# Performance work log

Hardware: AMD Instinct MI355X
Metric: run time of the kernel (lower is better)

The kernel has to match this reference:

```python
import jax, jax.numpy as jnp
import numpy as np

B, CIN, NH, W, L, K = 16, 64, 64, 32, 4, 5
EPS = 1e-5
FORGET_BIAS = 1.0


def conv(x, w, b=None):
    # x: [B,C,H,W], w: [O,I,k,k] -> SAME padding, stride 1 (NCHW)
    y = jax.lax.conv_general_dilated(x, w, (1, 1), 'SAME',
                                     dimension_numbers=('NCHW', 'OIHW', 'NCHW'))
    if b is not None:
        y = y + b[None, :, None, None]
    return y


def ln(x, g, b):
    # torch LayerNorm([C,W,W]): normalize each sample over (C,H,W)
    m = jnp.mean(x, axis=(1, 2, 3), keepdims=True)
    v = jnp.mean((x - m) ** 2, axis=(1, 2, 3), keepdims=True)
    return (x - m) * jax.lax.rsqrt(v + EPS) * g[None] + b[None]


def attn_channel(q, kv):
    # q: [B,C,W,H], kv: [B,L,C,W,H]
    b, c, w, h = q.shape
    qf = q.reshape(b, c, w * h)                 # [B,C,HW]
    kf = kv.reshape(b, -1, w * h)               # [B,L*C,HW]
    a = jax.nn.softmax(jnp.einsum('bcp,blp->bcl', qf, kf), axis=2)  # [B,C,L*C]
    out = jnp.einsum('bcl,blp->bcp', a, kf)     # [B,C,HW]
    return out.reshape(b, c, w, h)


def attn_spatial(q, kv):
    # q: [B,C,W,H], kv: [B,L,C,W,H]
    b, c, w, h = q.shape
    qf = q.reshape(b, c, w * h).transpose(0, 2, 1)          # [B,HW,C]
    kf = kv.transpose(0, 1, 3, 4, 2).reshape(b, -1, c)      # [B,L*HW,C]
    a = jax.nn.softmax(jnp.einsum('bpc,bqc->bpq', qf, kf), axis=2)  # [B,HW,L*HW]
    out = jnp.einsum('bpq,bqc->bpc', a, kf)                 # [B,HW,C]
    return out.reshape(b, w, h, c).transpose(0, 3, 1, 2)


def setup_inputs() -> dict:
    key = jax.random.key(0)
    ks = iter(jax.random.split(key, 64))
    rn = lambda shape, s=1.0: jax.random.normal(next(ks), shape, jnp.float32) * s
    ones = lambda shape: jnp.ones(shape, jnp.float32)
    zeros = lambda shape: jnp.zeros(shape, jnp.float32)
    s = 0.02
    d = {}
    d['x_t'] = rn((B, CIN, W, W))
    d['h_t'] = rn((B, NH, W, W))
    d['c_t'] = rn((B, NH, W, W))
    d['c_historys'] = rn((B, L, NH, W, W))
    d['m_t'] = rn((B, NH, W, W))
    d['w_x'] = rn((7 * NH, CIN, K, K), s); d['ln_x_g'] = ones((7 * NH, W, W)); d['ln_x_b'] = zeros((7 * NH, W, W))
    d['w_h'] = rn((4 * NH, NH, K, K), s);  d['ln_h_g'] = ones((4 * NH, W, W)); d['ln_h_b'] = zeros((4 * NH, W, W))
    d['w_m'] = rn((3 * NH, NH, K, K), s);  d['ln_m_g'] = ones((3 * NH, W, W)); d['ln_m_b'] = zeros((3 * NH, W, W))
    d['w_o'] = rn((NH, 2 * NH, K, K), s);  d['ln_o_g'] = ones((NH, W, W));     d['ln_o_b'] = zeros((NH, W, W))
    d['w_last'] = rn((NH, 2 * NH, 1, 1), s)
    d['s_norm_g'] = ones((NH, W, W)); d['s_norm_b'] = zeros((NH, W, W))
    d['c_norm_g'] = ones((NH, W, W)); d['c_norm_b'] = zeros((NH, W, W))
    d['ca_w1'] = rn((NH, NH, K, K), s); d['ca_b1'] = zeros((NH,))
    d['ca_ln_g'] = ones((NH, W, W));    d['ca_ln_b'] = zeros((NH, W, W))
    d['ca_w2'] = rn((NH, NH, 1, 1), s); d['ca_b2'] = zeros((NH,))
    d['sa_w1'] = rn((NH, NH, K, K), s)
    d['sa_ln_g'] = ones((NH, W, W));    d['sa_ln_b'] = zeros((NH, W, W))
    d['sa_w2'] = rn((NH, NH, 1, 1), s)
    d['attn_w'] = rn((NH, NH, 1, 1), s)
    return d


def reference(x_t, h_t, c_t, c_historys, m_t,
              w_x, ln_x_g, ln_x_b, w_h, ln_h_g, ln_h_b, w_m, ln_m_g, ln_m_b,
              w_o, ln_o_g, ln_o_b, w_last,
              s_norm_g, s_norm_b, c_norm_g, c_norm_b,
              ca_w1, ca_b1, ca_ln_g, ca_ln_b, ca_w2, ca_b2,
              sa_w1, sa_ln_g, sa_ln_b, sa_w2, attn_w):
    x_concat = ln(conv(x_t, w_x), ln_x_g, ln_x_b)
    h_concat = ln(conv(h_t, w_h), ln_h_g, ln_h_b)
    m_concat = ln(conv(m_t, w_m), ln_m_g, ln_m_b)
    (i_x, f_x, g_x, i_xp, f_xp, g_xp, o_x) = jnp.split(x_concat, 7, axis=1)
    (i_h, f_h, g_h, o_h) = jnp.split(h_concat, 4, axis=1)
    (i_m, f_m, g_m) = jnp.split(m_concat, 3, axis=1)

    i_t = jax.nn.sigmoid(i_x + i_h)
    f_t = jax.nn.sigmoid(f_x + f_h + FORGET_BIAS)
    g_t = jnp.tanh(g_x + g_h)

    # attn_sum_fussion(c_t, query=f_t, keys=c_historys, values=c_historys)
    sp = ln(c_t + attn_spatial(f_t, c_historys), s_norm_g, s_norm_b)
    ch = ln(c_t + attn_channel(f_t, c_historys), c_norm_g, c_norm_b)
    s_a = conv(jax.nn.relu(ln(conv(sp, sa_w1), sa_ln_g, sa_ln_b)), sa_w2)
    c_a = conv(jax.nn.relu(ln(conv(ch, ca_w1, ca_b1), ca_ln_g, ca_ln_b)), ca_w2, ca_b2)
    attn = conv(s_a + c_a, attn_w)
    c_new = attn + i_t * g_t

    i_tp = jax.nn.sigmoid(i_xp + i_m)
    f_tp = jax.nn.sigmoid(f_xp + f_m + FORGET_BIAS)
    g_tp = jnp.tanh(g_xp + g_m)
    m_new = f_tp * m_t + i_tp * g_tp

    mem = jnp.concatenate((c_new, m_new), axis=1)
    o_t = jax.nn.sigmoid(o_x + o_h + ln(conv(mem, w_o), ln_o_g, ln_o_b))
    h_new = o_t * jnp.tanh(conv(mem, w_last))
    return h_new, c_new, m_new
```

## Files before the change

kernel.cpp:

```cpp
#include <hip/hip_runtime.h>
#include <hip/hip_bf16.h>

#define N1 (1u << 20)

typedef __attribute__((ext_vector_type(8))) short s8v;
typedef __attribute__((ext_vector_type(4))) float f4v;

static __device__ __forceinline__ float sigm(float x){ return 1.f/(1.f + __expf(-x)); }
static __device__ __forceinline__ float tanh_(float x){ return 1.f - 2.f/(__expf(2.f*x) + 1.f); }

static __device__ __forceinline__ ushort f2b(float f){
  union { float f; uint u; } x; x.f = f;
  uint r = x.u + 0x7FFFu + ((x.u >> 16) & 1u);
  return (ushort)(r >> 16);
}

static __device__ __forceinline__ void red_atomic2(float s, float q, float* d, int b, int t){
  #pragma unroll
  for (int m = 32; m; m >>= 1){ s += __shfl_xor(s, m); q += __shfl_xor(q, m); }
  if ((t & 63) == 0){ atomicAdd(&d[b*2], s); atomicAdd(&d[b*2+1], q); }
}

__global__ void k_zero(float* __restrict__ p){ p[threadIdx.x] = 0.f; }

__global__ __launch_bounds__(256) void k_wprep3(
    const float* __restrict__ sA, ushort* __restrict__ dA, int CoA, int CiA, int nA,
    const float* __restrict__ sB, ushort* __restrict__ dB, int CoB, int CiB, int nB,
    const float* __restrict__ sC, ushort* __restrict__ dC, int CoC, int CiC, int nC)
{
  int idx = blockIdx.x*256 + threadIdx.x;
  const float* s; ushort* d; int Co, Ci;
  if (idx < nA){ s=sA; d=dA; Co=CoA; Ci=CiA; }
  else if ((idx -= nA) < nB){ s=sB; d=dB; Co=CoB; Ci=CiB; }
  else if ((idx -= nB) < nC){ s=sC; d=dC; Co=CoC; Ci=CiC; }
  else return;
  int ci = idx % Ci; int r = idx / Ci; int co = r % Co; int tap = r / Co;
  d[idx] = f2b(s[((size_t)(co*Ci + ci))*25 + tap]);
}

struct PT { const float* s; ushort* d; const float* st; const float* g; const float* bb; };

__global__ __launch_bounds__(256) void k_prepT3(PT ja, PT jb, PT jc, int n0, int n1, float invN)
{
  const int lp = blockIdx.y;
  PT j; int pl;
  if (lp < n0){ j = ja; pl = lp; }
  else if (lp < n0 + n1){ j = jb; pl = lp - n0; }
  else { j = jc; pl = lp - n0 - n1; }
  const float* sp = j.s + ((size_t)pl << 16);
  float mean = 0.f, rstd = 0.f;
  if (j.st){
    float s0 = j.st[pl*2], s1 = j.st[pl*2+1];
    mean = s0*invN; rstd = rsqrtf(s1*invN - mean*mean + 1e-5f);
  }
  const int p0 = blockIdx.x << 6;
  __shared__ __align__(16) float T[64][68];
  const int t = threadIdx.x, c = t >> 2, g4 = t & 3;
  #pragma unroll
  for (int i = 0; i < 4; ++i){
    const int px = (g4 << 4) + (i << 2);
    float4 f = *(const float4*)(sp + ((size_t)c << 10) + p0 + px);
    if (j.st){
      const size_t li = ((size_t)c << 10) + p0 + px;
      float4 gv = *(const float4*)(j.g + li);
      float4 bv = *(const float4*)(j.bb + li);
      f.x = (f.x - mean)*rstd*gv.x + bv.x;
      f.y = (f.y - mean)*rstd*gv.y + bv.y;
      f.z = (f.z - mean)*rstd*gv.z + bv.z;
      f.w = (f.w - mean)*rstd*gv.w + bv.w;
    }
    *(float4*)&T[c][px] = f;
  }
  __syncthreads();
  const int p = t >> 2, c0 = (t & 3) << 4;
  uint w4[8];
  #pragma unroll
  for (int k = 0; k < 8; ++k){
    ushort lo = f2b(T[c0 + 2*k][p]);
    ushort hi = f2b(T[c0 + 2*k + 1][p]);
    w4[k] = (uint)lo | ((uint)hi << 16);
  }
  ushort* dst = j.d + ((((size_t)pl << 10) + p0 + p) << 6) + c0;
  *(uint4*)(dst)     = *(uint4*)&w4[0];
  *(uint4*)(dst + 8) = *(uint4*)&w4[4];
}

__global__ __launch_bounds__(256) void k_prepTm(const float* __restrict__ src, ushort* __restrict__ dT)
{
  const int lp = blockIdx.y;
  const int p0 = blockIdx.x << 6;
  const float* sp = src + ((size_t)lp << 16);
  __shared__ __align__(16) float T[64][68];
  const int t = threadIdx.x, c = t >> 2, g4 = t & 3;
  #pragma unroll
  for (int i = 0; i < 4; ++i){
    const int px = (g4 << 4) + (i << 2);
    *(float4*)&T[c][px] = *(const float4*)(sp + ((size_t)c << 10) + p0 + px);
  }
  __syncthreads();
  const int p = t >> 2, c0 = (t & 3) << 4;
  uint w4[8];
  #pragma unroll
  for (int k = 0; k < 8; ++k)
    w4[k] = (uint)f2b(T[c0 + 2*k][p]) | ((uint)f2b(T[c0 + 2*k + 1][p]) << 16);
  ushort* dst = dT + ((((size_t)(lp >> 1) << 10) + p0 + p) << 7) + ((lp & 1) << 6) + c0;
  *(uint4*)(dst)     = *(uint4*)&w4[0];
  *(uint4*)(dst + 8) = *(uint4*)&w4[4];
}

struct Seg {
  const ushort* inT; const ushort* w; const float* bias;
  float* out; float* ostat;
  int Cin, Cout;
};
struct Segs3 { Seg s[3]; int b1, b2; };

template<int MT>
__global__ __launch_bounds__(256, MT==4 ? 2 : 3) void k_convX(Segs3 Sg)
{
  constexpr int CO   = MT*16;
  constexpr int NW   = 5*CO*4;
  constexpr int ITW  = (NW + 255) / 256;
  constexpr int DXSH = (MT == 4 ? 8 : 7);

  const int b = blockIdx.y;
  const int cog = blockIdx.x >> 2, pxblk = blockIdx.x & 3;
  const int si = (cog >= Sg.b1) + (cog >= Sg.b2);
  const Seg sg = Sg.s[si];
  const int base = si == 0 ? 0 : (si == 1 ? Sg.b1 : Sg.b2);
  const int co0 = (cog - base) * CO;
  const int r0 = pxblk << 3;
  const int t = threadIdx.x, w = t >> 6, l = t & 63;
  const int lane16 = l & 15, quad = l >> 4;

  __shared__ __align__(16) ushort S_[4][12][36][8];
  __shared__ __align__(16) ushort W_[2][5*CO*32];

  f4v acc[MT][4];
  #pragma unroll
  for (int mi = 0; mi < MT; ++mi)
    #pragma unroll
    for (int n = 0; n < 4; ++n) acc[mi][n] = (f4v){0.f,0.f,0.f,0.f};

  size_t woff0[ITW];
  #pragma unroll
  for (int it = 0; it < ITW; ++it){
    const int u = t + it*256;
    const int l16u = u & 15, qu = (u >> 4) & 3;
    const int miu = (u >> 6) & (MT - 1), dxu = u >> DXSH;
    woff0[it] = ((size_t)(dxu*sg.Cout + co0 + miu*16 + l16u))*sg.Cin + (qu << 3);
  }
  const size_t wdy = (size_t)5 * sg.Cout * sg.Cin;

  const int ncc = sg.Cin >> 5;
  for (int cc = 0; cc < ncc; ++cc){
    __syncthreads();
    for (int idx = t; idx < 432; idx += 256){
      const int row = idx / 36, col = idx - row*36;
      const int ir = r0 - 2 + row, ic = col - 2;
      uint4 pk[4] = {make_uint4(0,0,0,0),make_uint4(0,0,0,0),make_uint4(0,0,0,0),make_uint4(0,0,0,0)};
      if ((unsigned)ir < 32u && (unsigned)ic < 32u){
        const ushort* bp = sg.inT + ((size_t)((b << 10) + (ir << 5) + ic)) * sg.Cin + (cc << 5);
        #pragma unroll
        for (int q = 0; q < 4; ++q) pk[q] = *(const uint4*)(bp + (q << 3));
      }
      #pragma unroll
      for (int q = 0; q < 4; ++q) *(uint4*)&S_[q][row][col][0] = pk[q];
    }
    {
      uint4 wreg[ITW];
      #pragma unroll
      for (int it = 0; it < ITW; ++it)
        if (ITW*256 == NW || t + it*256 < NW)
          wreg[it] = *(const uint4*)(sg.w + woff0[it] + (cc << 5));
      #pragma unroll
      for (int it = 0; it < ITW; ++it)
        if (ITW*256 == NW || t + it*256 < NW)
          *(uint4*)&W_[0][(size_t)(t + it*256) * 8] = wreg[it];
    }
    __syncthreads();
    #pragma unroll
    for (int dy = 0; dy < 5; ++dy){
      uint4 nreg[ITW];
      if (dy < 4){
        #pragma unroll
        for (int it = 0; it < ITW; ++it)
          if (ITW*256 == NW || t + it*256 < NW)
            nreg[it] = *(const uint4*)(sg.w + woff0[it] + (size_t)(dy+1)*wdy + (cc << 5));
      }
      #pragma unroll
      for (int dx = 0; dx < 5; ++dx){
        s8v a[MT];
        #pragma unroll
        for (int mi = 0; mi < MT; ++mi){
          const int au = ((((dx*MT + mi) << 2) + quad) << 4) + lane16;
          a[mi] = *(const s8v*)&W_[dy & 1][au << 3];
        }
        #pragma unroll
        for (int n = 0; n < 4; ++n){
          const int srow = (w << 1) + (n >> 1) + dy;
          const int col = ((n & 1) << 4) + lane16 + dx;
          s8v bb = *(const s8v*)&S_[quad][srow][col][0];
          #pragma unroll
          for (int mi = 0; mi < MT; ++mi)
            acc[mi][n] = __builtin_amdgcn_mfma_f32_16x16x32_bf16(a[mi], bb, acc[mi][n], 0, 0, 0);
        }
      }
      if (dy < 4){
        #pragma unroll
        for (int it = 0; it < ITW; ++it)
          if (ITW*256 == NW || t + it*256 < NW)
            *(uint4*)&W_[(dy+1) & 1][(size_t)(t + it*256) * 8] = nreg[it];
      }
      __syncthreads();
    }
  }
  float lsum = 0.f, lsq = 0.f;
  #pragma unroll
  for (int mi = 0; mi < MT; ++mi){
    const int co = co0 + mi*16 + (quad << 2);
    #pragma unroll
    for (int n = 0; n < 4; ++n){
      const int row = r0 + (w << 1) + (n >> 1);
      const int col = ((n & 1) << 4) + lane16;
      #pragma unroll
      for (int i = 0; i < 4; ++i){
        float v = acc[mi][n][i] + (sg.bias ? sg.bias[co+i] : 0.f);
        sg.out[(((size_t)(b*sg.Cout + co + i)) << 10) + (row << 5) + col] = v;
        lsum += v; lsq += v*v;
      }
    }
  }
  if (sg.ostat) red_atomic2(lsum, lsq, sg.ostat, b, t);
}

__global__ __launch_bounds__(256) void k_prep(const float* __restrict__ src,
                                              ushort* __restrict__ outC,
                                              ushort* __restrict__ outT)
{
  const int plane = blockIdx.y;
  const int p0 = blockIdx.x << 6;
  const float* sp = src + ((size_t)plane << 16);
  __shared__ __align__(16) float T[64][68];
  const int t = threadIdx.x, c = t >> 2, g = t & 3;
  #pragma unroll
  for (int i = 0; i < 4; ++i){
    float4 f = *(const float4*)(sp + ((size_t)c << 10) + p0 + (g << 4) + (i << 2));
    *(float4*)&T[c][(g << 4) + (i << 2)] = f;
    if (outC){
      uint2 pk2;
      pk2.x = (uint)f2b(f.x) | ((uint)f2b(f.y) << 16);
      pk2.y = (uint)f2b(f.z) | ((uint)f2b(f.w) << 16);
      *(uint2*)(outC + ((((size_t)plane << 6) + c) << 10) + p0 + (g << 4) + (i << 2)) = pk2;
    }
  }
  __syncthreads();
  const int p = t >> 2, c0 = (t & 3) << 4;
  uint w4[8];
  #pragma unroll
  for (int k = 0; k < 8; ++k){
    ushort lo = f2b(T[c0 + 2*k][p]);
    ushort hi = f2b(T[c0 + 2*k + 1][p]);
    w4[k] = (uint)lo | ((uint)hi << 16);
  }
  ushort* dst = outT + ((((size_t)plane << 10) + p0 + p) << 6) + c0;
  *(uint4*)(dst)     = *(uint4*)&w4[0];
  *(uint4*)(dst + 8) = *(uint4*)&w4[4];
}

__global__ __launch_bounds__(256) void k_gates(
    const float* __restrict__ bufx, const float* __restrict__ bufh, const float* __restrict__ bufm,
    const float* __restrict__ lnxg, const float* __restrict__ lnxb,
    const float* __restrict__ lnhg, const float* __restrict__ lnhb,
    const float* __restrict__ lnmg, const float* __restrict__ lnmb,
    const float* __restrict__ m_t, const float* __restrict__ stats,
    float* __restrict__ ft, float* __restrict__ ig, float* __restrict__ osum,
    float* __restrict__ memo, float* __restrict__ out_m)
{
  const int idx = blockIdx.x*256 + threadIdx.x;
  const int b = idx >> 16, rem = idx & 65535;
  const int c = rem >> 10, p = rem & 1023;

  float mx = stats[b*2]      * (1.f/458752.f);
  float vx = stats[b*2+1]    * (1.f/458752.f) - mx*mx;  float rx = rsqrtf(vx + 1e-5f);
  float mh = stats[32+b*2]   * (1.f/262144.f);
  float vh = stats[32+b*2+1] * (1.f/262144.f) - mh*mh;  float rh = rsqrtf(vh + 1e-5f);
  float mm = stats[64+b*2]   * (1.f/196608.f);
  float vm = stats[64+b*2+1] * (1.f/196608.f) - mm*mm;  float rm = rsqrtf(vm + 1e-5f);

  auto LX = [&](int k){
    size_t ch = (size_t)k*64 + c; size_t gi = ((size_t)b*448 + ch)*1024 + p; size_t li = ch*1024 + p;
    return (bufx[gi] - mx)*rx*lnxg[li] + lnxb[li]; };
  auto LH = [&](int k){
    size_t ch = (size_t)k*64 + c; size_t gi = ((size_t)b*256 + ch)*1024 + p; size_t li = ch*1024 + p;
    return (bufh[gi] - mh)*rh*lnhg[li] + lnhb[li]; };
  auto LM = [&](int k){
    size_t ch = (size_t)k*64 + c; size_t gi = ((size_t)b*192 + ch)*1024 + p; size_t li = ch*1024 + p;
    return (bufm[gi] - mm)*rm*lnmg[li] + lnmb[li]; };

  float i_t = sigm(LX(0) + LH(0));
  float f_t = sigm(LX(1) + LH(1) + 1.f);
  float g_t = tanh_(LX(2) + LH(2));
  float i_p = sigm(LX(3) + LM(0));
  float f_p = sigm(LX(4) + LM(1) + 1.f);
  float g_p = tanh_(LX(5) + LM(2));
  float ox = LX(6), oh = LH(3);

  ft[idx]   = f_t;
  ig[idx]   = i_t * g_t;
  osum[idx] = ox + oh;
  float mn = f_p * m_t[idx] + i_p * g_p;
  out_m[idx] = mn;
  memo[((size_t)(b*128 + 64 + c) << 10) + p] = mn;
}

__global__ __launch_bounds__(256) void k_spat_mfma(
    const ushort* __restrict__ qT, const ushort* __restrict__ kvC, const ushort* __restrict__ kvT,
    const float* __restrict__ c_t, float* __restrict__ sp_raw, float* __restrict__ stats)
{
  const int p0 = blockIdx.x << 6, b = blockIdx.y;
  const int t = threadIdx.x, w = t >> 6, l = t & 63;
  const int lane16 = l & 15, quad = l >> 4;
  __shared__ __align__(16) ushort Kt[64][72];
  __shared__ __align__(16) ushort Kc[64][72];
  __shared__ __align__(16) ushort Eb[64][72];
  __shared__ __align__(16) float  XO[64][65];

  s8v qa0, qa1;
  {
    const ushort* qr = qT + ((((size_t)b << 10) + p0 + (w << 4) + lane16) << 6) + (quad << 3);
    qa0 = *(const s8v*)(qr);
    qa1 = *(const s8v*)(qr + 32);
  }
  f4v o0 = {0.f,0.f,0.f,0.f}, o1 = o0, o2 = o0, o3 = o0, dacc = o0;
  const short oneb = (short)0x3F80;
  const s8v ones = { oneb, oneb, oneb, oneb, oneb, oneb, oneb, oneb };

  const int r = t >> 2, g4 = (t & 3) << 4;
  for (int chunk = 0; chunk < 64; ++chunk){
    const int lidx = chunk >> 4, pk = (chunk & 15) << 6;
    __syncthreads();
    {
      const ushort* sc = kvC + ((((size_t)(b*4 + lidx) << 6) + r) << 10) + pk + g4;
      *(uint4*)&Kc[r][g4]     = *(const uint4*)(sc);
      *(uint4*)&Kc[r][g4 + 8] = *(const uint4*)(sc + 8);
      const ushort* st = kvT + ((((size_t)(b*4 + lidx) << 10) + pk + r) << 6) + g4;
      *(uint4*)&Kt[r][g4]     = *(const uint4*)(st);
      *(uint4*)&Kt[r][g4 + 8] = *(const uint4*)(st + 8);
    }
    __syncthreads();
    #pragma unroll
    for (int nt = 0; nt < 4; ++nt){
      const ushort* bt = &Kt[(nt << 4) + lane16][quad << 3];
      s8v b0 = *(const s8v*)(bt);
      s8v b1 = *(const s8v*)(bt + 32);
      f4v s = {0.f,0.f,0.f,0.f};
      s = __builtin_amdgcn_mfma_f32_16x16x32_bf16(qa0, b0, s, 0, 0, 0);
      s = __builtin_amdgcn_mfma_f32_16x16x32_bf16(qa1, b1, s, 0, 0, 0);
      #pragma unroll
      for (int i = 0; i < 4; ++i){
        float e = __expf(s[i] - 12.f);
        Eb[(w << 4) + (quad << 2) + i][(nt << 4) + lane16] = f2b(e);
      }
    }
    __syncthreads();
    #pragma unroll
    for (int ks = 0; ks < 2; ++ks){
      s8v ea = *(const s8v*)&Eb[(w << 4) + lane16][(ks << 5) + (quad << 3)];
      dacc = __builtin_amdgcn_mfma_f32_16x16x32_bf16(ea, ones, dacc, 0, 0, 0);
      s8v bc0 = *(const s8v*)&Kc[ 0 + lane16][(ks << 5) + (quad << 3)];
      s8v bc1 = *(const s8v*)&Kc[16 + lane16][(ks << 5) + (quad << 3)];
      s8v bc2 = *(const s8v*)&Kc[32 + lane16][(ks << 5) + (quad << 3)];
      s8v bc3 = *(const s8v*)&Kc[48 + lane16][(ks << 5) + (quad << 3)];
      o0 = __builtin_amdgcn_mfma_f32_16x16x32_bf16(ea, bc0, o0, 0, 0, 0);
      o1 = __builtin_amdgcn_mfma_f32_16x16x32_bf16(ea, bc1, o1, 0, 0, 0);
      o2 = __builtin_amdgcn_mfma_f32_16x16x32_bf16(ea, bc2, o2, 0, 0, 0);
      o3 = __builtin_amdgcn_mfma_f32_16x16x32_bf16(ea, bc3, o3, 0, 0, 0);
    }
  }
  {
    float inv0 = 1.f/dacc[0], inv1 = 1.f/dacc[1], inv2 = 1.f/dacc[2], inv3 = 1.f/dacc[3];
    const int pxl = (w << 4) + (quad << 2);
    XO[ 0 + lane16][pxl+0] = o0[0]*inv0; XO[ 0 + lane16][pxl+1] = o0[1]*inv1;
    XO[ 0 + lane16][pxl+2] = o0[2]*inv2; XO[ 0 + lane16][pxl+3] = o0[3]*inv3;
    XO[16 + lane16][pxl+0] = o1[0]*inv0; XO[16 + lane16][pxl+1] = o1[1]*inv1;
    XO[16 + lane16][pxl+2] = o1[2]*inv2; XO[16 + lane16][pxl+3] = o1[3]*inv3;
    XO[32 + lane16][pxl+0] = o2[0]*inv0; XO[32 + lane16][pxl+1] = o2[1]*inv1;
    XO[32 + lane16][pxl+2] = o2[2]*inv2; XO[32 + lane16][pxl+3] = o2[3]*inv3;
    XO[48 + lane16][pxl+0] = o3[0]*inv0; XO[48 + lane16][pxl+1] = o3[1]*inv1;
    XO[48 + lane16][pxl+2] = o3[2]*inv2; XO[48 + lane16][pxl+3] = o3[3]*inv3;
  }
  __syncthreads();
  {
    const int ch = t >> 2;
    float lsum = 0.f, lsq = 0.f;
    #pragma unroll
    for (int i = 0; i < 4; ++i){
      size_t gi = ((size_t)b << 16) + ((size_t)ch << 10) + p0 + g4 + (i << 2);
      float4 cv = *(const float4*)(c_t + gi);
      float4 ov;
      ov.x = cv.x + XO[ch][g4 + (i << 2) + 0];
      ov.y = cv.y + XO[ch][g4 + (i << 2) + 1];
      ov.z = cv.z + XO[ch][g4 + (i << 2) + 2];
      ov.w = cv.w + XO[ch][g4 + (i << 2) + 3];
      *(float4*)(sp_raw + gi) = ov;
      lsum += ov.x + ov.y + ov.z + ov.w;
      lsq  += ov.x*ov.x + ov.y*ov.y + ov.z*ov.z + ov.w*ov.w;
    }
    red_atomic2(lsum, lsq, stats, b, t);
  }
}

__global__ __launch_bounds__(256) void k_chlog_m(
    const ushort* __restrict__ ftC, const ushort* __restrict__ kvC, float* __restrict__ lg)
{
  const int lp = blockIdx.x, b = blockIdx.y;
  const int t = threadIdx.x, w = t >> 6, l = t & 63;
  const int lane16 = l & 15, quad = l >> 4;
  __shared__ __align__(16) ushort As[8][64][8];
  __shared__ __align__(16) ushort Bs[8][128][8];
  f4v acc[4][2];
  #pragma unroll
  for (int mi = 0; mi < 4; ++mi){ acc[mi][0] = (f4v){0.f,0.f,0.f,0.f}; acc[mi][1] = (f4v){0.f,0.f,0.f,0.f}; }

  for (int kc = 0; kc < 16; ++kc){
    __syncthreads();
    #pragma unroll
    for (int it = 0; it < 2; ++it){
      const int idx = t + it*256;
      const int c = idx >> 3, q = idx & 7;
      *(uint4*)&As[q][c][0] = *(const uint4*)(ftC + (((size_t)(b*64 + c)) << 10) + (kc<<6) + (q<<3));
    }
    #pragma unroll
    for (int it = 0; it < 4; ++it){
      const int idx = t + it*256;
      const int r2 = idx >> 3, q = idx & 7;
      const int plane = (b<<2) + (lp<<1) + (r2>>6);
      *(uint4*)&Bs[q][r2][0] = *(const uint4*)(kvC + ((((size_t)plane << 6) + (r2 & 63)) << 10) + (kc<<6) + (q<<3));
    }
    __syncthreads();
    #pragma unroll
    for (int ks = 0; ks < 2; ++ks){
      s8v a[4];
      #pragma unroll
      for (int mi = 0; mi < 4; ++mi)
        a[mi] = *(const s8v*)&As[(ks<<2)+quad][mi*16 + lane16][0];
      #pragma unroll
      for (int nt = 0; nt < 2; ++nt){
        s8v bb = *(const s8v*)&Bs[(ks<<2)+quad][(w<<5) + (nt<<4) + lane16][0];
        #pragma unroll
        for (int mi = 0; mi < 4; ++mi)
          acc[mi][nt] = __builtin_amdgcn_mfma_f32_16x16x32_bf16(a[mi], bb, acc[mi][nt], 0, 0, 0);
      }
    }
  }
  #pragma unroll
  for (int mi = 0; mi < 4; ++mi)
    #pragma unroll
    for (int nt = 0; nt < 2; ++nt)
      #pragma unroll
      for (int i = 0; i < 4; ++i){
        const int c = mi*16 + (quad<<2) + i;
        const int n = (lp<<7) + (w<<5) + (nt<<4) + lane16;
        lg[(((size_t)(b*64 + c)) << 8) + n] = acc[mi][nt][i];
      }
}

__global__ __launch_bounds__(256) void k_chsm(const float* __restrict__ a, ushort* __restrict__ ab)
{
  const int row  = blockIdx.x*4 + (threadIdx.x >> 6);
  const int lane = threadIdx.x & 63;
  const float* rp = a + ((size_t)row << 8);
  float v0 = rp[lane], v1 = rp[lane+64], v2 = rp[lane+128], v3 = rp[lane+192];
  float mx = fmaxf(fmaxf(v0, v1), fmaxf(v2, v3));
  #pragma unroll
  for (int m = 32; m; m >>= 1) mx = fmaxf(mx, __shfl_xor(mx, m));
  v0 = __expf(v0 - mx); v1 = __expf(v1 - mx); v2 = __expf(v2 - mx); v3 = __expf(v3 - mx);
  float s = v0 + v1 + v2 + v3;
  #pragma unroll
  for (int m = 32; m; m >>= 1) s += __shfl_xor(s, m);
  float inv = 1.f / s;
  ushort* op = ab + ((size_t)row << 8);
  op[lane] = f2b(v0*inv); op[lane+64] = f2b(v1*inv);
  op[lane+128] = f2b(v2*inv); op[lane+192] = f2b(v3*inv);
}

__global__ __launch_bounds__(256) void k_chout_m(
    const ushort* __restrict__ chlb, const ushort* __restrict__ kvT,
    const float* __restrict__ c_t, float* __restrict__ ch_raw, float* __restrict__ stats)
{
  const int p0 = blockIdx.x << 7, b = blockIdx.y;
  const int t = threadIdx.x, w = t >> 6, l = t & 63;
  const int lane16 = l & 15, quad = l >> 4;
  __shared__ __align__(16) ushort As[32][64][8];
  __shared__ __align__(16) ushort Bs[32][32][8];
  #pragma unroll
  for (int it = 0; it < 8; ++it){
    const int idx = t + it*256;
    const int c = idx >> 5, q = idx & 31;
    *(uint4*)&As[q][c][0] = *(const uint4*)(chlb + (((size_t)(b*64 + c)) << 8) + (q<<3));
  }
  __syncthreads();
  s8v a[8];
  #pragma unroll
  for (int ks = 0; ks < 8; ++ks)
    a[ks] = *(const s8v*)&As[(ks<<2)+quad][(w<<4) + lane16][0];
  float lsum = 0.f, lsq = 0.f;
  for (int pc = 0; pc < 4; ++pc){
    __syncthreads();
    #pragma unroll
    for (int it = 0; it < 4; ++it){
      const int idx = t + it*256;
      const int px = idx >> 5, q = idx & 31;
      const int plane = (b<<2) + (q>>3);
      *(uint4*)&Bs[q][px][0] = *(const uint4*)(kvT + ((((size_t)plane << 10) + p0 + (pc<<5) + px) << 6) + ((q&7)<<3));
    }
    __syncthreads();
    #pragma unroll
    for (int nt = 0; nt < 2; ++nt){
      f4v o = {0.f,0.f,0.f,0.f};
      #pragma unroll
      for (int ks = 0; ks < 8; ++ks){
        s8v bb = *(const s8v*)&Bs[(ks<<2)+quad][(nt<<4) + lane16][0];
        o = __builtin_amdgcn_mfma_f32_16x16x32_bf16(a[ks], bb, o, 0, 0, 0);
      }
      #pragma unroll
      for (int i = 0; i < 4; ++i){
        const int c = (w<<4) + (quad<<2) + i;
        const int px = p0 + (pc<<5) + (nt<<4) + lane16;
        size_t gi = ((size_t)b << 16) + ((size_t)c << 10) + px;
        float v = c_t[gi] + o[i];
        ch_raw[gi] = v;
        lsum += v; lsq += v*v;
      }
    }
  }
  red_atomic2(lsum, lsq, stats, b, t);
}

__global__ __launch_bounds__(256) void k_attnfinal(
    const float* __restrict__ samid, const float* __restrict__ camid,
    const float* __restrict__ stats_sa, const float* __restrict__ stats_ca,
    const float* __restrict__ salng, const float* __restrict__ salnb,
    const float* __restrict__ calng, const float* __restrict__ calnb,
    const float* __restrict__ wsa2, const float* __restrict__ wca2,
    const float* __restrict__ cab2, const float* __restrict__ wat,
    const float* __restrict__ ig, float* __restrict__ out_c, float* __restrict__ memo)
{
  const int p0 = blockIdx.x << 6, b = blockIdx.y, t = threadIdx.x;
  const int tc = t & 15, tp = t >> 4;
  __shared__ __align__(16) float R[64][68];
  __shared__ __align__(16) float Wl[64][68];
  __shared__ __align__(16) float Ms[64][68];
  const float invN = 1.f/65536.f;
  float acc[4][4] = {};
  #pragma unroll
  for (int pass = 0; pass < 2; ++pass){
    const float* mid = pass ? camid : samid;
    const float* st  = pass ? stats_ca : stats_sa;
    const float* g   = pass ? calng : salng;
    const float* bb  = pass ? calnb : salnb;
    const float* w   = pass ? wca2  : wsa2;
    float mean = st[b*2]*invN;
    float var  = st[b*2+1]*invN - mean*mean;
    float rstd = rsqrtf(var + 1e-5f);
    __syncthreads();
    {
      const int j = t & 63, c0 = t >> 6;
      for (int ci = c0; ci < 64; ci += 4){
        size_t gi = ((size_t)b << 16) + ((size_t)ci << 10) + p0 + j;
        size_t li = ((size_t)ci << 10) + p0 + j;
        float v = (mid[gi] - mean)*rstd*g[li] + bb[li];
        R[ci][j] = fmaxf(v, 0.f);
      }
      const int ci2 = t & 63, c20 = t >> 6;
      for (int c2 = c20; c2 < 64; c2 += 4) Wl[ci2][c2] = w[((size_t)c2 << 6) + ci2];
    }
    __syncthreads();
    for (int ci = 0; ci < 64; ++ci){
      float wv[4], rv[4];
      *(float4*)wv = *(const float4*)&Wl[ci][4*tc];
      *(float4*)rv = *(const float4*)&R[ci][4*tp];
      #pragma unroll
      for (int i = 0; i < 4; ++i)
        #pragma unroll
        for (int j = 0; j < 4; ++j)
          acc[i][j] = fmaf(wv[i], rv[j], acc[i][j]);
    }
  }
  {
    float b2[4];
    #pragma unroll
    for (int i = 0; i < 4; ++i) b2[i] = cab2[4*tc + i];
    #pragma unroll
    for (int i = 0; i < 4; ++i)
      #pragma unroll
      for (int j = 0; j < 4; ++j)
        Ms[4*tc+i][4*tp+j] = acc[i][j] + b2[i];
  }
  __syncthreads();
  {
    const int ci2 = t & 63, c20 = t >> 6;
    for (int c2 = c20; c2 < 64; c2 += 4) Wl[ci2][c2] = wat[((size_t)c2 << 6) + ci2];
  }
  __syncthreads();
  float acc2[4][4] = {};
  for (int c2 = 0; c2 < 64; ++c2){
    float wv[4], mv[4];
    *(float4*)wv = *(const float4*)&Wl[c2][4*tc];
    *(float4*)mv = *(const float4*)&Ms[c2][4*tp];
    #pragma unroll
    for (int i = 0; i < 4; ++i)
      #pragma unroll
      for (int j = 0; j < 4; ++j)
        acc2[i][j] = fmaf(wv[i], mv[j], acc2[i][j]);
  }
  #pragma unroll
  for (int i = 0; i < 4; ++i)
    #pragma unroll
    for (int j = 0; j < 4; ++j){
      size_t gi = ((size_t)b << 16) + ((size_t)(4*tc + i) << 10) + p0 + 4*tp + j;
      float v = acc2[i][j] + ig[gi];
      out_c[gi] = v;
      memo[((size_t)(b*128 + 4*tc + i) << 10) + p0 + 4*tp + j] = v;
    }
}

__global__ __launch_bounds__(256) void k_final(
    const float* __restrict__ memo, const float* __restrict__ wlast,
    const float* __restrict__ bufo, const float* __restrict__ osum,
    const float* __restrict__ stats_o, const float* __restrict__ lnog, const float* __restrict__ lnob,
    float* __restrict__ out_h)
{
  const int p0 = blockIdx.x << 6, b = blockIdx.y, t = threadIdx.x;
  const int tc = t & 15, tp = t >> 4;
  __shared__ __align__(16) float Msh[64][68];
  __shared__ __align__(16) float Wt[64][68];
  float acc[4][4] = {};
  #pragma unroll
  for (int half = 0; half < 2; ++half){
    __syncthreads();
    {
      const int j = t & 63, c0 = t >> 6;
      for (int ci = c0; ci < 64; ci += 4)
        Msh[ci][j] = memo[((size_t)(b*128 + half*64 + ci) << 10) + p0 + j];
      const int ci2 = t & 63, co0 = t >> 6;
      for (int co = co0; co < 64; co += 4) Wt[ci2][co] = wlast[((size_t)co << 7) + half*64 + ci2];
    }
    __syncthreads();
    for (int ci = 0; ci < 64; ++ci){
      float wv[4], mv[4];
      *(float4*)wv = *(const float4*)&Wt[ci][4*tc];
      *(float4*)mv = *(const float4*)&Msh[ci][4*tp];
      #pragma unroll
      for (int i = 0; i < 4; ++i)
        #pragma unroll
        for (int j = 0; j < 4; ++j)
          acc[i][j] = fmaf(wv[i], mv[j], acc[i][j]);
    }
  }
  float mean = stats_o[b*2]*(1.f/65536.f);
  float var  = stats_o[b*2+1]*(1.f/65536.f) - mean*mean;
  float rstd = rsqrtf(var + 1e-5f);
  #pragma unroll
  for (int i = 0; i < 4; ++i)
    #pragma unroll
    for (int j = 0; j < 4; ++j){
      const int co = 4*tc + i, p = p0 + 4*tp + j;
      size_t gi = ((size_t)b << 16) + ((size_t)co << 10) + p;
      size_t li = ((size_t)co << 10) + p;
      float lno = (bufo[gi] - mean)*rstd*lnog[li] + lnob[li];
      float o = sigm(osum[gi] + lno);
      out_h[gi] = o * tanh_(acc[i][j]);
    }
}

extern "C" void kernel_launch(void* const* d_in, const int* in_sizes, int n_in,
                              void* d_out, int out_size, void* d_ws, size_t ws_size,
                              hipStream_t stream)
{
  const float* x_t   = (const float*)d_in[0];
  const float* h_t   = (const float*)d_in[1];
  const float* c_t   = (const float*)d_in[2];
  const float* chist = (const float*)d_in[3];
  const float* m_t   = (const float*)d_in[4];
  const float* w_x   = (const float*)d_in[5];
  const float* lnxg  = (const float*)d_in[6];
  const float* lnxb  = (const float*)d_in[7];
  const float* w_h   = (const float*)d_in[8];
  const float* lnhg  = (const float*)d_in[9];
  const float* lnhb  = (const float*)d_in[10];
  const float* w_m   = (const float*)d_in[11];
  const float* lnmg  = (const float*)d_in[12];
  const float* lnmb  = (const float*)d_in[13];
  const float* w_o   = (const float*)d_in[14];
  const float* lnog  = (const float*)d_in[15];
  const float* lnob  = (const float*)d_in[16];
  const float* w_last= (const float*)d_in[17];
  const float* sng   = (const float*)d_in[18];
  const float* snb   = (const float*)d_in[19];
  const float* cng   = (const float*)d_in[20];
  const float* cnb   = (const float*)d_in[21];
  const float* ca_w1 = (const float*)d_in[22];
  const float* ca_b1 = (const float*)d_in[23];
  const float* calng = (const float*)d_in[24];
  const float* calnb = (const float*)d_in[25];
  const float* ca_w2 = (const float*)d_in[26];
  const float* ca_b2 = (const float*)d_in[27];
  const float* sa_w1 = (const float*)d_in[28];
  const float* salng = (const float*)d_in[29];
  const float* salnb = (const float*)d_in[30];
  const float* sa_w2 = (const float*)d_in[31];
  const float* attn_w= (const float*)d_in[32];

  float* out = (float*)d_out;
  float* ws  = (float*)d_ws;

  float* stats = ws;
  float* bufx  = ws + 1024;
  float* bufh  = bufx + 7*(size_t)N1;
  float* bufm  = bufh + 4*(size_t)N1;
  float* ft    = bufm + 3*(size_t)N1;
  float* ig    = ft   + (size_t)N1;
  float* osum  = ig   + (size_t)N1;
  float* memo  = osum + (size_t)N1;
  float* sp    = bufx;
  float* ch    = bufx + (size_t)N1;
  float* samid = bufx + 2*(size_t)N1;
  float* camid = bufx + 3*(size_t)N1;
  float* bufo  = bufx + 4*(size_t)N1;
  float* chl   = bufx + 5*(size_t)N1;
  ushort* kvC  = (ushort*)bufh;
  ushort* kvT  = kvC + 4*(size_t)N1;
  ushort* qT   = (ushort*)bufm;
  ushort* ftC  = qT + (size_t)N1;

  ushort* xT   = (ushort*)memo;
  ushort* hT   = xT + (size_t)N1;
  ushort* mT   = hT + (size_t)N1;
  ushort* spT  = ftC + (size_t)N1;
  ushort* chT  = spT + (size_t)N1;
  ushort* memoT = (ushort*)bufx;

  ushort* wbx = (ushort*)ft;
  ushort* wbh = wbx + 716800;
  ushort* wbm = wbh + 409600;
  ushort* wbo  = (ushort*)(chl + 262144);
  ushort* wbsa = wbo + 204800;
  ushort* wbca = wbsa + 102400;
  ushort* chlb = wbca + 102400;

  float* out_h = out;
  float* out_c = out + (size_t)N1;
  float* out_m = out + 2*(size_t)N1;

  k_zero<<<dim3(1), dim3(256), 0, stream>>>(stats);

  k_wprep3<<<dim3(5600), dim3(256), 0, stream>>>(
      w_x, wbx, 448, 64, 716800,
      w_h, wbh, 256, 64, 409600,
      w_m, wbm, 192, 64, 307200);

  {
    PT jx{ x_t, xT, nullptr, nullptr, nullptr };
    PT jh{ h_t, hT, nullptr, nullptr, nullptr };
    PT jm{ m_t, mT, nullptr, nullptr, nullptr };
    k_prepT3<<<dim3(16,48), dim3(256), 0, stream>>>(jx, jh, jm, 16, 16, 0.f);
  }

  {
    Segs3 XHM;
    XHM.s[0] = Seg{ xT, wbx, nullptr, bufx, stats+0,  64, 448 };
    XHM.s[1] = Seg{ hT, wbh, nullptr, bufh, stats+32, 64, 256 };
    XHM.s[2] = Seg{ mT, wbm, nullptr, bufm, stats+64, 64, 192 };
    XHM.b1 = 7; XHM.b2 = 11;
    k_convX<4><<<dim3(56,16), dim3(256), 0, stream>>>(XHM);
  }

  k_gates<<<dim3(4096), dim3(256), 0, stream>>>(bufx, bufh, bufm, lnxg, lnxb, lnhg, lnhb,
                                                lnmg, lnmb, m_t, stats,
                                                ft, ig, osum, memo, out_m);

  k_wprep3<<<dim3(1600), dim3(256), 0, stream>>>(
      w_o,   wbo,  64, 128, 204800,
      sa_w1, wbsa, 64,  64, 102400,
      ca_w1, wbca, 64,  64, 102400);

  k_prep<<<dim3(16,64), dim3(256), 0, stream>>>(chist, kvC, kvT);
  k_prep<<<dim3(16,16), dim3(256), 0, stream>>>(ft, ftC, qT);

  k_spat_mfma<<<dim3(16,16), dim3(256), 0, stream>>>(qT, kvC, kvT, c_t, sp, stats+96);
  k_chlog_m<<<dim3(2,16), dim3(256), 0, stream>>>(ftC, kvC, chl);
  k_chsm  <<<dim3(256),  dim3(256), 0, stream>>>(chl, chlb);
  k_chout_m<<<dim3(8,16), dim3(256), 0, stream>>>(chlb, kvT, c_t, ch, stats+128);

  {
    PT js{ sp, spT, stats+96,  sng, snb };
    PT jc{ ch, chT, stats+128, cng, cnb };
    k_prepT3<<<dim3(16,32), dim3(256), 0, stream>>>(js, jc, js, 16, 16, 1.f/65536.f);
  }

  {
    Segs3 SC;
    SC.s[0] = Seg{ spT, wbsa, nullptr, samid, stats+160, 64, 64 };
    SC.s[1] = Seg{ chT, wbca, ca_b1,   camid, stats+192, 64, 64 };
    SC.s[2] = SC.s[1];
    SC.b1 = 2; SC.b2 = 1000;
    k_convX<2><<<dim3(16,16), dim3(256), 0, stream>>>(SC);
  }

  k_attnfinal<<<dim3(16,16), dim3(256), 0, stream>>>(samid, camid, stats+160, stats+192,
                                                     salng, salnb, calng, calnb,
                                                     sa_w2, ca_w2, ca_b2, attn_w,
                                                     ig, out_c, memo);

  k_prepTm<<<dim3(16,32), dim3(256), 0, stream>>>(memo, memoT);

  {
    Segs3 O;
    O.s[0] = Seg{ memoT, wbo, nullptr, bufo, stats+224, 128, 64 };
    O.s[1] = O.s[0]; O.s[2] = O.s[0];
    O.b1 = 1000; O.b2 = 1000;
    k_convX<2><<<dim3(8,16), dim3(256), 0, stream>>>(O);
  }

  k_final<<<dim3(16,16), dim3(256), 0, stream>>>(memo, w_last, bufo, osum, stats+224,
                                                 lnog, lnob, out_h);
}
```

Baseline: 519.0 us.

## Split spatial attention over key halves and retile channel-attention kernels for more blocks

The spatial attention kernel now splits its 64 key chunks across two blocks per tile. Each block writes an unnormalised numerator and a denominator partial, and a new k_spcomb kernel sums the two halves, divides, adds c_t and accumulates the LayerNorm statistics. The channel-logit kernel is retiled into smaller 32x64 output tiles, giving 128 blocks instead of 32, and the channel-output kernel processes 64 pixels per block, doubling its grid. The goal is to fill more compute units on small grids. The cost is one extra launch and a round trip of partial results through global memory.

```diff
diff --git a/kernel.cpp b/kernel.cpp
--- a/kernel.cpp
+++ b/kernel.cpp
@@ -316,9 +316,9 @@
 
 __global__ __launch_bounds__(256) void k_spat_mfma(
     const ushort* __restrict__ qT, const ushort* __restrict__ kvC, const ushort* __restrict__ kvT,
-    const float* __restrict__ c_t, float* __restrict__ sp_raw, float* __restrict__ stats)
-{
-  const int p0 = blockIdx.x << 6, b = blockIdx.y;
+    float* __restrict__ num0, float* __restrict__ num1, float* __restrict__ den)
+{
+  const int p0 = blockIdx.x << 6, b = blockIdx.y, half = blockIdx.z;
   const int t = threadIdx.x, w = t >> 6, l = t & 63;
   const int lane16 = l & 15, quad = l >> 4;
   __shared__ __align__(16) ushort Kt[64][72];
@@ -337,7 +337,8 @@
   const s8v ones = { oneb, oneb, oneb, oneb, oneb, oneb, oneb, oneb };
 
   const int r = t >> 2, g4 = (t & 3) << 4;
-  for (int chunk = 0; chunk < 64; ++chunk){
+  for (int ck = 0; ck < 32; ++ck){
+    const int chunk = (half << 5) + ck;
     const int lidx = chunk >> 4, pk = (chunk & 15) << 6;
     __syncthreads();
     {
@@ -379,91 +380,107 @@
     }
   }
   {
-    float inv0 = 1.f/dacc[0], inv1 = 1.f/dacc[1], inv2 = 1.f/dacc[2], inv3 = 1.f/dacc[3];
     const int pxl = (w << 4) + (quad << 2);
-    XO[ 0 + lane16][pxl+0] = o0[0]*inv0; XO[ 0 + lane16][pxl+1] = o0[1]*inv1;
-    XO[ 0 + lane16][pxl+2] = o0[2]*inv2; XO[ 0 + lane16][pxl+3] = o0[3]*inv3;
-    XO[16 + lane16][pxl+0] = o1[0]*inv0; XO[16 + lane16][pxl+1] = o1[1]*inv1;
-    XO[16 + lane16][pxl+2] = o1[2]*inv2; XO[16 + lane16][pxl+3] = o1[3]*inv3;
-    XO[32 + lane16][pxl+0] = o2[0]*inv0; XO[32 + lane16][pxl+1] = o2[1]*inv1;
-    XO[32 + lane16][pxl+2] = o2[2]*inv2; XO[32 + lane16][pxl+3] = o2[3]*inv3;
-    XO[48 + lane16][pxl+0] = o3[0]*inv0; XO[48 + lane16][pxl+1] = o3[1]*inv1;
-    XO[48 + lane16][pxl+2] = o3[2]*inv2; XO[48 + lane16][pxl+3] = o3[3]*inv3;
+    if (lane16 == 0){
+      float* dp = den + (((size_t)(half*16 + b)) << 10) + p0 + pxl;
+      dp[0] = dacc[0]; dp[1] = dacc[1]; dp[2] = dacc[2]; dp[3] = dacc[3];
+    }
+    XO[ 0 + lane16][pxl+0] = o0[0]; XO[ 0 + lane16][pxl+1] = o0[1];
+    XO[ 0 + lane16][pxl+2] = o0[2]; XO[ 0 + lane16][pxl+3] = o0[3];
+    XO[16 + lane16][pxl+0] = o1[0]; XO[16 + lane16][pxl+1] = o1[1];
+    XO[16 + lane16][pxl+2] = o1[2]; XO[16 + lane16][pxl+3] = o1[3];
+    XO[32 + lane16][pxl+0] = o2[0]; XO[32 + lane16][pxl+1] = o2[1];
+    XO[32 + lane16][pxl+2] = o2[2]; XO[32 + lane16][pxl+3] = o2[3];
+    XO[48 + lane16][pxl+0] = o3[0]; XO[48 + lane16][pxl+1] = o3[1];
+    XO[48 + lane16][pxl+2] = o3[2]; XO[48 + lane16][pxl+3] = o3[3];
   }
   __syncthreads();
   {
     const int ch = t >> 2;
-    float lsum = 0.f, lsq = 0.f;
+    float* nout = half ? num1 : num0;
     #pragma unroll
     for (int i = 0; i < 4; ++i){
       size_t gi = ((size_t)b << 16) + ((size_t)ch << 10) + p0 + g4 + (i << 2);
-      float4 cv = *(const float4*)(c_t + gi);
       float4 ov;
-      ov.x = cv.x + XO[ch][g4 + (i << 2) + 0];
-      ov.y = cv.y + XO[ch][g4 + (i << 2) + 1];
-      ov.z = cv.z + XO[ch][g4 + (i << 2) + 2];
-      ov.w = cv.w + XO[ch][g4 + (i << 2) + 3];
-      *(float4*)(sp_raw + gi) = ov;
-      lsum += ov.x + ov.y + ov.z + ov.w;
-      lsq  += ov.x*ov.x + ov.y*ov.y + ov.z*ov.z + ov.w*ov.w;
-    }
-    red_atomic2(lsum, lsq, stats, b, t);
-  }
+      ov.x = XO[ch][g4 + (i << 2) + 0];
+      ov.y = XO[ch][g4 + (i << 2) + 1];
+      ov.z = XO[ch][g4 + (i << 2) + 2];
+      ov.w = XO[ch][g4 + (i << 2) + 3];
+      *(float4*)(nout + gi) = ov;
+    }
+  }
+}
+
+__global__ __launch_bounds__(256) void k_spcomb(
+    const float* num0, const float* num1, const float* __restrict__ den,
+    const float* __restrict__ c_t, float* sp_raw, float* __restrict__ stats)
+{
+  const int p0 = blockIdx.x << 6, b = blockIdx.y, t = threadIdx.x;
+  const int ch = t >> 2, g4 = (t & 3) << 4;
+  float lsum = 0.f, lsq = 0.f;
+  #pragma unroll
+  for (int i = 0; i < 4; ++i){
+    const int px = p0 + g4 + (i << 2);
+    size_t gi = ((size_t)b << 16) + ((size_t)ch << 10) + px;
+    float4 n0 = *(const float4*)(num0 + gi);
+    float4 n1 = *(const float4*)(num1 + gi);
+    float4 cv = *(const float4*)(c_t + gi);
+    const float* d0 = den + (((size_t)b) << 10) + px;
+    const float* d1 = den + (((size_t)(16 + b)) << 10) + px;
+    float4 ov;
+    ov.x = cv.x + (n0.x + n1.x) / (d0[0] + d1[0]);
+    ov.y = cv.y + (n0.y + n1.y) / (d0[1] + d1[1]);
+    ov.z = cv.z + (n0.z + n1.z) / (d0[2] + d1[2]);
+    ov.w = cv.w + (n0.w + n1.w) / (d0[3] + d1[3]);
+    *(float4*)(sp_raw + gi) = ov;
+    lsum += ov.x + ov.y + ov.z + ov.w;
+    lsq  += ov.x*ov.x + ov.y*ov.y + ov.z*ov.z + ov.w*ov.w;
+  }
+  red_atomic2(lsum, lsq, stats, b, t);
 }
 
 __global__ __launch_bounds__(256) void k_chlog_m(
     const ushort* __restrict__ ftC, const ushort* __restrict__ kvC, float* __restrict__ lg)
 {
-  const int lp = blockIdx.x, b = blockIdx.y;
+  const int bx = blockIdx.x, b = blockIdx.y;
+  const int np = bx >> 1, mp = bx & 1;
   const int t = threadIdx.x, w = t >> 6, l = t & 63;
   const int lane16 = l & 15, quad = l >> 4;
-  __shared__ __align__(16) ushort As[8][64][8];
-  __shared__ __align__(16) ushort Bs[8][128][8];
-  f4v acc[4][2];
-  #pragma unroll
-  for (int mi = 0; mi < 4; ++mi){ acc[mi][0] = (f4v){0.f,0.f,0.f,0.f}; acc[mi][1] = (f4v){0.f,0.f,0.f,0.f}; }
+  __shared__ __align__(16) ushort As[8][32][8];
+  __shared__ __align__(16) ushort Bs[8][64][8];
+  f4v acc[2];
+  acc[0] = (f4v){0.f,0.f,0.f,0.f}; acc[1] = (f4v){0.f,0.f,0.f,0.f};
 
   for (int kc = 0; kc < 16; ++kc){
     __syncthreads();
+    {
+      const int c = t >> 3, q = t & 7;
+      *(uint4*)&As[q][c][0] = *(const uint4*)(ftC + (((size_t)(b*64 + mp*32 + c)) << 10) + (kc<<6) + (q<<3));
+    }
     #pragma unroll
     for (int it = 0; it < 2; ++it){
       const int idx = t + it*256;
-      const int c = idx >> 3, q = idx & 7;
-      *(uint4*)&As[q][c][0] = *(const uint4*)(ftC + (((size_t)(b*64 + c)) << 10) + (kc<<6) + (q<<3));
-    }
-    #pragma unroll
-    for (int it = 0; it < 4; ++it){
-      const int idx = t + it*256;
       const int r2 = idx >> 3, q = idx & 7;
-      const int plane = (b<<2) + (lp<<1) + (r2>>6);
-      *(uint4*)&Bs[q][r2][0] = *(const uint4*)(kvC + ((((size_t)plane << 6) + (r2 & 63)) << 10) + (kc<<6) + (q<<3));
+      *(uint4*)&Bs[q][r2][0] = *(const uint4*)(kvC + ((((size_t)(b*4 + np) << 6) + r2) << 10) + (kc<<6) + (q<<3));
     }
     __syncthreads();
     #pragma unroll
     for (int ks = 0; ks < 2; ++ks){
-      s8v a[4];
-      #pragma unroll
-      for (int mi = 0; mi < 4; ++mi)
-        a[mi] = *(const s8v*)&As[(ks<<2)+quad][mi*16 + lane16][0];
-      #pragma unroll
-      for (int nt = 0; nt < 2; ++nt){
-        s8v bb = *(const s8v*)&Bs[(ks<<2)+quad][(w<<5) + (nt<<4) + lane16][0];
-        #pragma unroll
-        for (int mi = 0; mi < 4; ++mi)
-          acc[mi][nt] = __builtin_amdgcn_mfma_f32_16x16x32_bf16(a[mi], bb, acc[mi][nt], 0, 0, 0);
-      }
-    }
-  }
-  #pragma unroll
-  for (int mi = 0; mi < 4; ++mi)
-    #pragma unroll
-    for (int nt = 0; nt < 2; ++nt)
-      #pragma unroll
-      for (int i = 0; i < 4; ++i){
-        const int c = mi*16 + (quad<<2) + i;
-        const int n = (lp<<7) + (w<<5) + (nt<<4) + lane16;
-        lg[(((size_t)(b*64 + c)) << 8) + n] = acc[mi][nt][i];
-      }
+      s8v a0 = *(const s8v*)&As[(ks<<2)+quad][lane16][0];
+      s8v a1 = *(const s8v*)&As[(ks<<2)+quad][16 + lane16][0];
+      s8v bb = *(const s8v*)&Bs[(ks<<2)+quad][(w<<4) + lane16][0];
+      acc[0] = __builtin_amdgcn_mfma_f32_16x16x32_bf16(a0, bb, acc[0], 0, 0, 0);
+      acc[1] = __builtin_amdgcn_mfma_f32_16x16x32_bf16(a1, bb, acc[1], 0, 0, 0);
+    }
+  }
+  #pragma unroll
+  for (int mi = 0; mi < 2; ++mi)
+    #pragma unroll
+    for (int i = 0; i < 4; ++i){
+      const int c = mp*32 + mi*16 + (quad<<2) + i;
+      const int n = (np<<6) + (w<<4) + lane16;
+      lg[(((size_t)(b*64 + c)) << 8) + n] = acc[mi][i];
+    }
 }
 
 __global__ __launch_bounds__(256) void k_chsm(const float* __restrict__ a, ushort* __restrict__ ab)
@@ -489,7 +506,7 @@
     const ushort* __restrict__ chlb, const ushort* __restrict__ kvT,
     const float* __restrict__ c_t, float* __restrict__ ch_raw, float* __restrict__ stats)
 {
-  const int p0 = blockIdx.x << 7, b = blockIdx.y;
+  const int p0 = blockIdx.x << 6, b = blockIdx.y;
   const int t = threadIdx.x, w = t >> 6, l = t & 63;
   const int lane16 = l & 15, quad = l >> 4;
   __shared__ __align__(16) ushort As[32][64][8];
@@ -506,7 +523,7 @@
   for (int ks = 0; ks < 8; ++ks)
     a[ks] = *(const s8v*)&As[(ks<<2)+quad][(w<<4) + lane16][0];
   float lsum = 0.f, lsq = 0.f;
-  for (int pc = 0; pc < 4; ++pc){
+  for (int pc = 0; pc < 2; ++pc){
     __syncthreads();
     #pragma unroll
     for (int it = 0; it < 4; ++it){
@@ -740,6 +757,8 @@
   ushort* mT   = hT + (size_t)N1;
   ushort* spT  = ftC + (size_t)N1;
   ushort* chT  = spT + (size_t)N1;
+  float*  num1 = bufm + 2*(size_t)N1;
+  float*  denP = chl;
   ushort* memoT = (ushort*)bufx;
 
   ushort* wbx = (ushort*)ft;
@@ -789,10 +808,12 @@
   k_prep<<<dim3(16,64), dim3(256), 0, stream>>>(chist, kvC, kvT);
   k_prep<<<dim3(16,16), dim3(256), 0, stream>>>(ft, ftC, qT);
 
-  k_spat_mfma<<<dim3(16,16), dim3(256), 0, stream>>>(qT, kvC, kvT, c_t, sp, stats+96);
-  k_chlog_m<<<dim3(2,16), dim3(256), 0, stream>>>(ftC, kvC, chl);
+  k_spat_mfma<<<dim3(16,16,2), dim3(256), 0, stream>>>(qT, kvC, kvT, sp, num1, denP);
+  k_spcomb<<<dim3(16,16), dim3(256), 0, stream>>>(sp, num1, denP, c_t, sp, stats+96);
+
+  k_chlog_m<<<dim3(8,16), dim3(256), 0, stream>>>(ftC, kvC, chl);
   k_chsm  <<<dim3(256),  dim3(256), 0, stream>>>(chl, chlb);
-  k_chout_m<<<dim3(8,16), dim3(256), 0, stream>>>(chlb, kvT, c_t, ch, stats+128);
+  k_chout_m<<<dim3(16,16), dim3(256), 0, stream>>>(chlb, kvT, c_t, ch, stats+128);
 
   {
     PT js{ sp, spT, stats+96,  sng, snb };
```

New measurement: 496.8 us. -4.3%, faster.
